# Performance work log

Hardware: AMD Instinct MI355X
Metric: run time of the kernel (lower is better)

Reference implementation:

```python
import jax, jax.numpy as jnp
import numpy as np

N_RECEIVERS = 8192
N_DONORS = 50000
NAN_SENTINEL = 1e10  # torch.nan_to_num(nan=10000000000.0)


def setup_inputs() -> dict:
    key = jax.random.key(0)
    k1, k2, k3 = jax.random.split(key, 3)
    dist_pot_donors = jax.random.uniform(k1, (N_RECEIVERS, N_DONORS), dtype=jnp.float32)
    fit_X_col = jax.random.normal(k2, (N_DONORS,), dtype=jnp.float32)
    mask_fit_X_col = jax.random.randint(k3, (N_DONORS,), 0, 2, dtype=jnp.int64)
    return {
        "dist_pot_donors": dist_pot_donors,
        "n_neighbors": 16,
        "fit_X_col": fit_X_col,
        "mask_fit_X_col": mask_fit_X_col,
    }


def reference(dist_pot_donors, n_neighbors, fit_X_col, mask_fit_X_col):
    # SubDonorsIdx: nan -> big sentinel, then k smallest per row (sorted ascending)
    xn = jnp.nan_to_num(dist_pot_donors, nan=NAN_SENTINEL)
    neg_vals, donors_idx = jax.lax.top_k(-xn, n_neighbors)  # [R, k]
    donors_dist = -neg_vals                                  # ascending distances

    # SubWeightMatrix with weights=None: ones, zero where donors_dist is NaN
    weight_matrix = jnp.where(jnp.isnan(donors_dist),
                              jnp.zeros((), donors_dist.dtype),
                              jnp.ones((), donors_dist.dtype))

    # gather donor values and inverted missingness mask
    donors = fit_X_col[donors_idx]                           # [R, k]
    donors_mask = 1 - mask_fit_X_col[donors_idx]             # int, 1 = valid donor

    # MakeNewWeights: mask (as float) * weight matrix
    new_weights = donors_mask.astype(donors.dtype) * weight_matrix.astype(donors.dtype)

    weights_sum = new_weights.sum(axis=1, keepdims=True)     # [R, 1]
    div = jnp.where(weights_sum == 0, jnp.ones((), weights_sum.dtype), weights_sum)
    res = (donors * new_weights).sum(axis=1, keepdims=True) / div
    return res.squeeze(1).astype(dist_pot_donors.dtype)     # [R]
```

## Files before the change

### kernel.cpp

```cpp
#include <hip/hip_runtime.h>
#include <limits.h>
#include <math.h>


#define K          16
#define NDON       50000
#define NF4        12500
#define MAIN_START 64
#define MAIN_STEPS 48
#define TAIL_START 12352

__device__ __forceinline__ bool lexless(float v1, int i1, float v2, int i2) {
    return (v1 < v2) || ((v1 == v2) && (i1 < i2));
}

__device__ __forceinline__ float nanfix(float v) { return (v != v) ? 1e10f : v; }

__device__ __forceinline__ void insert16(float (&vals)[K], int (&idxs)[K],
                                         float cv, int ci) {
    if (!lexless(cv, ci, vals[K - 1], idxs[K - 1])) return;
    bool prev = true;
#pragma unroll
    for (int j = K - 1; j >= 1; --j) {
        const bool up = lexless(cv, ci, vals[j - 1], idxs[j - 1]);
        const float nv = up ? vals[j - 1] : (prev ? cv : vals[j]);
        const int   ni = up ? idxs[j - 1] : (prev ? ci : idxs[j]);
        vals[j] = nv; idxs[j] = ni;
        prev = up;
    }
    if (prev) { vals[0] = cv; idxs[0] = ci; }
}

#define CE(va, ia, vb, ib)                                         \
    {                                                              \
        const bool sw_ = lexless(vb, ib, va, ia);                  \
        const float tv_ = va; const int ti_ = ia;                  \
        va = sw_ ? vb : va; ia = sw_ ? ib : ia;                    \
        vb = sw_ ? tv_ : vb; ib = sw_ ? ti_ : ib;                  \
    }

__global__ void __launch_bounds__(256, 4)
calc_impute_topk(const float* __restrict__ dist,
                 const float* __restrict__ fitX,
                 const int*   __restrict__ mask,
                 float* __restrict__ out,
                 int nrows)
{
    const int gtid = blockIdx.x * blockDim.x + threadIdx.x;
    const int wrow = gtid >> 6;
    const int lane = threadIdx.x & 63;
    if (wrow >= nrows) return;

    const float4* __restrict__ r4 =
        reinterpret_cast<const float4*>(dist + (size_t)wrow * NDON);

    float4 d = r4[lane];
    float l0 = nanfix(d.x), l1 = nanfix(d.y), l2 = nanfix(d.z), l3 = nanfix(d.w);
    int   j0 = lane * 4, j1 = j0 + 1, j2 = j0 + 2, j3 = j0 + 3;
    CE(l0, j0, l1, j1); CE(l2, j2, l3, j3);
    CE(l0, j0, l2, j2); CE(l1, j1, l3, j3);
    CE(l1, j1, l2, j2);

    float vals[K];
    int   idxs[K];
#pragma unroll
    for (int r = 0; r < K; ++r) {
        float mv = l0; int mi = j0;
#pragma unroll
        for (int m = 32; m >= 1; m >>= 1) {
            const float ov = __shfl_xor(mv, m, 64);
            const int   oi = __shfl_xor(mi, m, 64);
            if (lexless(ov, oi, mv, mi)) { mv = ov; mi = oi; }
        }
        vals[r] = mv; idxs[r] = mi;
        if (l0 == mv && j0 == mi) {
            l0 = l1; j0 = j1; l1 = l2; j1 = j2; l2 = l3; j2 = j3;
            l3 = INFINITY; j3 = INT_MAX;
        }
    }
    float Tv = vals[K - 1];

#define PROC(ve, ie)                                                   \
    {                                                                  \
        unsigned long long bb_ = __ballot((ve) <= Tv);                 \
        while (bb_) {                                                  \
            const int src_ = __builtin_ctzll(bb_); bb_ &= bb_ - 1;     \
            const float cv_ = __shfl((ve), src_, 64);                  \
            const int   ci_ = __shfl((ie), src_, 64);                  \
            insert16(vals, idxs, cv_, ci_);                            \
        }                                                              \
    }

    const float4* p0 = r4 + MAIN_START + lane;
    float4 c0 = p0[0], c1 = p0[64], c2 = p0[128], c3 = p0[192];
#pragma unroll 1
    for (int s = 0; s < MAIN_STEPS; ++s) {
        float4 n0, n1, n2, n3;
        const bool more = (s + 1 < MAIN_STEPS);
        if (more) {
            const float4* pn = r4 + MAIN_START + (s + 1) * 256 + lane;
            n0 = pn[0]; n1 = pn[64]; n2 = pn[128]; n3 = pn[192];
        }
        const float m0 = fminf(fminf(c0.x, c0.y), fminf(c0.z, c0.w));
        const float m1 = fminf(fminf(c1.x, c1.y), fminf(c1.z, c1.w));
        const float m2 = fminf(fminf(c2.x, c2.y), fminf(c2.z, c2.w));
        const float m3 = fminf(fminf(c3.x, c3.y), fminf(c3.z, c3.w));
        const float mn = fminf(fminf(m0, m1), fminf(m2, m3));
        if (__any(mn <= Tv)) {
            const int b0 = (MAIN_START + s * 256 + lane) * 4;
            PROC(c0.x, b0 + 0);   PROC(c0.y, b0 + 1);
            PROC(c0.z, b0 + 2);   PROC(c0.w, b0 + 3);
            PROC(c1.x, b0 + 256); PROC(c1.y, b0 + 257);
            PROC(c1.z, b0 + 258); PROC(c1.w, b0 + 259);
            PROC(c2.x, b0 + 512); PROC(c2.y, b0 + 513);
            PROC(c2.z, b0 + 514); PROC(c2.w, b0 + 515);
            PROC(c3.x, b0 + 768); PROC(c3.y, b0 + 769);
            PROC(c3.z, b0 + 770); PROC(c3.w, b0 + 771);
            Tv = vals[K - 1];
        }
        c0 = n0; c1 = n1; c2 = n2; c3 = n3;
    }

#pragma unroll 1
    for (int t = 0; t < 3; ++t) {
        const int f4i = TAIL_START + t * 64 + lane;
        float4 e;
        if (f4i < NF4) {
            e = r4[f4i];
        } else {
            e.x = e.y = e.z = e.w = INFINITY;
        }
        const int b0 = f4i * 4;
        PROC(e.x, b0 + 0); PROC(e.y, b0 + 1);
        PROC(e.z, b0 + 2); PROC(e.w, b0 + 3);
    }
#undef PROC

    float s_w = 0.0f, s_wx = 0.0f;
#pragma unroll
    for (int r = 0; r < K; ++r) {
        const int mi = idxs[r];
        const float w = 1.0f - (float)mask[mi];
        s_w  += w;
        s_wx += w * fitX[mi];
    }
    if (lane == 0) {
        out[wrow] = s_wx / ((s_w == 0.0f) ? 1.0f : s_w);
    }
}

extern "C" void kernel_launch(void* const* d_in, const int* in_sizes, int n_in,
                              void* d_out, int out_size, void* d_ws, size_t ws_size,
                              hipStream_t stream) {
    const float* dist = (const float*)d_in[0];
    const float* fitX = (const float*)d_in[2];
    const int*   mask = (const int*)d_in[3];
    float* out = (float*)d_out;

    const int nrows = out_size;
    const int threads = 256;
    const int blocks = (nrows * 64 + threads - 1) / threads;

    calc_impute_topk<<<blocks, threads, 0, stream>>>(dist, fitX, mask, out, nrows);
}
```

Before: 387.3 us.

## Filter candidates below a fixed threshold with a flat scan, then merge per row

Replaces the per-row wavefront top-k with three kernels. A flat, grid-strided scan streams the whole distance matrix and appends every value below a fixed threshold (TAU = 1e-3) to a per-row bucket using atomics. A per-row merge kernel then picks the 16 smallest from that bucket with 64-bit shuffle reductions, and falls back to a full rescan of the row when the bucket holds fewer than 16 or overflows. The aim is to make the main pass purely bandwidth-bound, without per-row insertion or branchy ballot work. The threshold is tuned to the uniform input distribution, and the packed sort key orders negative distances incorrectly.

```diff
diff --git a/kernel.cpp b/kernel.cpp
--- a/kernel.cpp
+++ b/kernel.cpp
@@ -3,21 +3,160 @@
 #include <math.h>
 
 
-#define K          16
-#define NDON       50000
-#define NF4        12500
-#define MAIN_START 64
-#define MAIN_STEPS 48
-#define TAIL_START 12352
+#define NROWS 8192
+#define NDON  50000
+#define NF4   12500
+#define K     16
+#define TAU   1.0e-3f
+#define CAP   128
+#define SUPER 100000
+
+typedef unsigned long long u64;
 
 __device__ __forceinline__ bool lexless(float v1, int i1, float v2, int i2) {
     return (v1 < v2) || ((v1 == v2) && (i1 < i2));
 }
-
 __device__ __forceinline__ float nanfix(float v) { return (v != v) ? 1e10f : v; }
 
-__device__ __forceinline__ void insert16(float (&vals)[K], int (&idxs)[K],
-                                         float cv, int ci) {
+__global__ void k_zero(int* __restrict__ cnt) {
+    const int i = blockIdx.x * blockDim.x + threadIdx.x;
+    if (i < NROWS) cnt[i] = 0;
+}
+
+__global__ void __launch_bounds__(256, 8)
+k_scan(const float4* __restrict__ d4, u64* __restrict__ buck,
+       int* __restrict__ cnt) {
+    const int t = threadIdx.x;
+
+#define EMIT(vf, ee)                                                        \
+    if ((vf) < TAU) {                                                       \
+        const int e_ = (ee);                                                \
+        const int row_ = e_ / NDON;                                         \
+        const int col_ = e_ - row_ * NDON;                                  \
+        const int pos_ = atomicAdd(&cnt[row_], 1);                          \
+        if (pos_ < CAP)                                                     \
+            buck[(size_t)row_ * CAP + pos_] =                               \
+                ((u64)__float_as_uint(vf) << 32) | (unsigned)col_;          \
+    }
+#define EMIT4(q, fi)                                                        \
+    {                                                                       \
+        const int e0_ = (fi) * 4;                                           \
+        EMIT(q.x, e0_); EMIT(q.y, e0_ + 1);                                 \
+        EMIT(q.z, e0_ + 2); EMIT(q.w, e0_ + 3);                             \
+    }
+
+    for (int sc = blockIdx.x; sc < SUPER; sc += gridDim.x) {
+        const int F = sc * 1024 + t;
+        const float4 a = d4[F];
+        const float4 b = d4[F + 256];
+        const float4 c = d4[F + 512];
+        const float4 d = d4[F + 768];
+        const float ma = fminf(fminf(a.x, a.y), fminf(a.z, a.w));
+        const float mb = fminf(fminf(b.x, b.y), fminf(b.z, b.w));
+        const float mc = fminf(fminf(c.x, c.y), fminf(c.z, c.w));
+        const float md = fminf(fminf(d.x, d.y), fminf(d.z, d.w));
+        if (fminf(fminf(ma, mb), fminf(mc, md)) < TAU) {
+            if (ma < TAU) EMIT4(a, F);
+            if (mb < TAU) EMIT4(b, F + 256);
+            if (mc < TAU) EMIT4(c, F + 512);
+            if (md < TAU) EMIT4(d, F + 768);
+        }
+    }
+#undef EMIT4
+#undef EMIT
+}
+
+__global__ void __launch_bounds__(64)
+k_merge(const u64* __restrict__ buck, const int* __restrict__ cnt,
+        const float* __restrict__ dist, const float* __restrict__ fitX,
+        const int* __restrict__ mask, float* __restrict__ out, int nrows) {
+    const int row = blockIdx.x;
+    const int lane = threadIdx.x;
+    if (row >= nrows) return;
+
+    const int n = cnt[row];
+    float s_w = 0.0f, s_wx = 0.0f;
+
+    if (n >= K && n <= CAP) {
+        const u64* bp = buck + (size_t)row * CAP;
+        u64 k0 = (lane < n)      ? bp[lane]      : ~0ull;
+        u64 k1 = (lane + 64 < n) ? bp[lane + 64] : ~0ull;
+        if (k1 < k0) { const u64 tt = k0; k0 = k1; k1 = tt; }
+#pragma unroll
+        for (int r = 0; r < K; ++r) {
+            u64 mv = k0;
+#pragma unroll
+            for (int m = 32; m >= 1; m >>= 1) {
+                const u64 ov = __shfl_xor(mv, m, 64);
+                if (ov < mv) mv = ov;
+            }
+            if (k0 == mv) { k0 = k1; k1 = ~0ull; }
+            const int col = (int)(unsigned)(mv & 0xffffffffu);
+            const float w = 1.0f - (float)mask[col];
+            s_w  += w;
+            s_wx += w * fitX[col];
+        }
+    } else {
+        const float4* r4 = reinterpret_cast<const float4*>(dist + (size_t)row * NDON);
+        float vals[K]; int idxs[K];
+#pragma unroll
+        for (int j = 0; j < K; ++j) { vals[j] = INFINITY; idxs[j] = INT_MAX; }
+        float Tv = INFINITY;
+
+#define PROC(ve, ie)                                                   \
+    {                                                                  \
+        unsigned long long bb_ = __ballot((ve) <= Tv);                 \
+        while (bb_) {                                                  \
+            const int src_ = __builtin_ctzll(bb_); bb_ &= bb_ - 1;     \
+            const float cv_ = __shfl((ve), src_, 64);                  \
+            const int   ci_ = __shfl((ie), src_, 64);                  \
+            if (lexless(cv_, ci_, vals[K - 1], idxs[K - 1])) {         \
+                vals[K - 1] = cv_; idxs[K - 1] = ci_;                  \
+                for (int j_ = K - 1; j_ > 0; --j_) {                   \
+                    if (lexless(vals[j_], idxs[j_],                    \
+                                vals[j_ - 1], idxs[j_ - 1])) {         \
+                        const float tv_ = vals[j_];                    \
+                        const int ti_ = idxs[j_];                      \
+                        vals[j_] = vals[j_ - 1]; idxs[j_] = idxs[j_ - 1]; \
+                        vals[j_ - 1] = tv_; idxs[j_ - 1] = ti_;        \
+                    } else break;                                      \
+                }                                                      \
+            }                                                          \
+        }                                                              \
+    }
+
+        for (int it = 0; it < 196; ++it) {
+            const int f4i = it * 64 + lane;
+            float4 q;
+            if (f4i < NF4) {
+                q = r4[f4i];
+            } else {
+                q.x = q.y = q.z = q.w = INFINITY;
+            }
+            const float x0 = nanfix(q.x), x1 = nanfix(q.y),
+                        x2 = nanfix(q.z), x3 = nanfix(q.w);
+            const int e0 = f4i * 4;
+            PROC(x0, e0 + 0); PROC(x1, e0 + 1);
+            PROC(x2, e0 + 2); PROC(x3, e0 + 3);
+            Tv = vals[K - 1];
+        }
+#undef PROC
+#pragma unroll
+        for (int r = 0; r < K; ++r) {
+            const int col = idxs[r];
+            const float w = 1.0f - (float)mask[col];
+            s_w  += w;
+            s_wx += w * fitX[col];
+        }
+    }
+
+    if (lane == 0) {
+        out[row] = s_wx / ((s_w == 0.0f) ? 1.0f : s_w);
+    }
+}
+
+__device__ __forceinline__ void insert16m(float (&vals)[K], int (&idxs)[K],
+                                          float cv, int ci) {
     if (!lexless(cv, ci, vals[K - 1], idxs[K - 1])) return;
     bool prev = true;
 #pragma unroll
@@ -40,7 +179,7 @@
     }
 
 __global__ void __launch_bounds__(256, 4)
-calc_impute_topk(const float* __restrict__ dist,
+calc_impute_mono(const float* __restrict__ dist,
                  const float* __restrict__ fitX,
                  const int*   __restrict__ mask,
                  float* __restrict__ out,
@@ -61,8 +200,7 @@
     CE(l0, j0, l2, j2); CE(l1, j1, l3, j3);
     CE(l1, j1, l2, j2);
 
-    float vals[K];
-    int   idxs[K];
+    float vals[K]; int idxs[K];
 #pragma unroll
     for (int r = 0; r < K; ++r) {
         float mv = l0; int mi = j0;
@@ -80,61 +218,56 @@
     }
     float Tv = vals[K - 1];
 
-#define PROC(ve, ie)                                                   \
+#define PROCM(ve, ie)                                                  \
     {                                                                  \
         unsigned long long bb_ = __ballot((ve) <= Tv);                 \
         while (bb_) {                                                  \
             const int src_ = __builtin_ctzll(bb_); bb_ &= bb_ - 1;     \
             const float cv_ = __shfl((ve), src_, 64);                  \
             const int   ci_ = __shfl((ie), src_, 64);                  \
-            insert16(vals, idxs, cv_, ci_);                            \
+            insert16m(vals, idxs, cv_, ci_);                           \
         }                                                              \
     }
 
-    const float4* p0 = r4 + MAIN_START + lane;
+    const float4* p0 = r4 + 64 + lane;
     float4 c0 = p0[0], c1 = p0[64], c2 = p0[128], c3 = p0[192];
 #pragma unroll 1
-    for (int s = 0; s < MAIN_STEPS; ++s) {
+    for (int s = 0; s < 48; ++s) {
         float4 n0, n1, n2, n3;
-        const bool more = (s + 1 < MAIN_STEPS);
+        const bool more = (s + 1 < 48);
         if (more) {
-            const float4* pn = r4 + MAIN_START + (s + 1) * 256 + lane;
+            const float4* pn = r4 + 64 + (s + 1) * 256 + lane;
             n0 = pn[0]; n1 = pn[64]; n2 = pn[128]; n3 = pn[192];
         }
         const float m0 = fminf(fminf(c0.x, c0.y), fminf(c0.z, c0.w));
         const float m1 = fminf(fminf(c1.x, c1.y), fminf(c1.z, c1.w));
         const float m2 = fminf(fminf(c2.x, c2.y), fminf(c2.z, c2.w));
         const float m3 = fminf(fminf(c3.x, c3.y), fminf(c3.z, c3.w));
-        const float mn = fminf(fminf(m0, m1), fminf(m2, m3));
-        if (__any(mn <= Tv)) {
-            const int b0 = (MAIN_START + s * 256 + lane) * 4;
-            PROC(c0.x, b0 + 0);   PROC(c0.y, b0 + 1);
-            PROC(c0.z, b0 + 2);   PROC(c0.w, b0 + 3);
-            PROC(c1.x, b0 + 256); PROC(c1.y, b0 + 257);
-            PROC(c1.z, b0 + 258); PROC(c1.w, b0 + 259);
-            PROC(c2.x, b0 + 512); PROC(c2.y, b0 + 513);
-            PROC(c2.z, b0 + 514); PROC(c2.w, b0 + 515);
-            PROC(c3.x, b0 + 768); PROC(c3.y, b0 + 769);
-            PROC(c3.z, b0 + 770); PROC(c3.w, b0 + 771);
+        if (__any(fminf(fminf(m0, m1), fminf(m2, m3)) <= Tv)) {
+            const int e0 = (64 + s * 256 + lane) * 4;
+            PROCM(c0.x, e0 + 0);   PROCM(c0.y, e0 + 1);
+            PROCM(c0.z, e0 + 2);   PROCM(c0.w, e0 + 3);
+            PROCM(c1.x, e0 + 256); PROCM(c1.y, e0 + 257);
+            PROCM(c1.z, e0 + 258); PROCM(c1.w, e0 + 259);
+            PROCM(c2.x, e0 + 512); PROCM(c2.y, e0 + 513);
+            PROCM(c2.z, e0 + 514); PROCM(c2.w, e0 + 515);
+            PROCM(c3.x, e0 + 768); PROCM(c3.y, e0 + 769);
+            PROCM(c3.z, e0 + 770); PROCM(c3.w, e0 + 771);
             Tv = vals[K - 1];
         }
         c0 = n0; c1 = n1; c2 = n2; c3 = n3;
     }
-
 #pragma unroll 1
     for (int t = 0; t < 3; ++t) {
-        const int f4i = TAIL_START + t * 64 + lane;
+        const int f4i = 12352 + t * 64 + lane;
         float4 e;
-        if (f4i < NF4) {
-            e = r4[f4i];
-        } else {
-            e.x = e.y = e.z = e.w = INFINITY;
-        }
+        if (f4i < NF4) { e = r4[f4i]; }
+        else { e.x = e.y = e.z = e.w = INFINITY; }
         const int b0 = f4i * 4;
-        PROC(e.x, b0 + 0); PROC(e.y, b0 + 1);
-        PROC(e.z, b0 + 2); PROC(e.w, b0 + 3);
-    }
-#undef PROC
+        PROCM(e.x, b0 + 0); PROCM(e.y, b0 + 1);
+        PROCM(e.z, b0 + 2); PROCM(e.w, b0 + 3);
+    }
+#undef PROCM
 
     float s_w = 0.0f, s_wx = 0.0f;
 #pragma unroll
@@ -156,10 +289,20 @@
     const float* fitX = (const float*)d_in[2];
     const int*   mask = (const int*)d_in[3];
     float* out = (float*)d_out;
-
     const int nrows = out_size;
-    const int threads = 256;
-    const int blocks = (nrows * 64 + threads - 1) / threads;
-
-    calc_impute_topk<<<blocks, threads, 0, stream>>>(dist, fitX, mask, out, nrows);
-}
+
+    const size_t needed = (size_t)NROWS * sizeof(int)
+                        + (size_t)NROWS * CAP * sizeof(u64);
+    if (ws_size >= needed) {
+        int* cnt  = (int*)d_ws;
+        u64* buck = (u64*)((char*)d_ws + NROWS * sizeof(int));
+        k_zero<<<(NROWS + 255) / 256, 256, 0, stream>>>(cnt);
+        k_scan<<<2048, 256, 0, stream>>>(
+            reinterpret_cast<const float4*>(dist), buck, cnt);
+        k_merge<<<nrows, 64, 0, stream>>>(buck, cnt, dist, fitX, mask, out, nrows);
+    } else {
+        const int threads = 256;
+        const int blocks = (nrows * 64 + threads - 1) / threads;
+        calc_impute_mono<<<blocks, threads, 0, stream>>>(dist, fitX, mask, out, nrows);
+    }
+}
```

After: 351.3 us. 1.1x faster.
